# Optimization experiments

Measured on AMD Instinct MI355X. Metric: run time of the kernel, lower is better.

## Reference

```python
import jax, jax.numpy as jnp
import numpy as np
from jax import lax

D, H, B, T = 128, 256, 64, 2048

def setup_inputs() -> dict:
    key = jax.random.key(0)
    k1, k2, k3, k4 = jax.random.split(key, 4)
    s_ih = 1.0 / np.sqrt(D)
    s_hh = 1.0 / np.sqrt(H)
    return {
        "inputs": jax.random.normal(k1, (B, T, D), dtype=jnp.float32),
        "W_ih": jax.random.normal(k2, (D, 4 * H), dtype=jnp.float32) * s_ih,
        "W_hh": jax.random.normal(k3, (H, 4 * H), dtype=jnp.float32) * s_hh,
        "b": jnp.zeros((4 * H,), dtype=jnp.float32),
        "W_out": jax.random.normal(k4, (H, 1), dtype=jnp.float32) * s_hh,
        "b_out": jnp.zeros((1,), dtype=jnp.float32),
    }

def _lstm_last_h(x_bt, W_ih, W_hh, b):
    # x_bt: [B, T, D] -> time-major [T, B, D]
    x = jnp.transpose(x_bt, (1, 0, 2))
    # precompute input projections as one big GEMM: [T, B, 4H]
    x_proj = jnp.einsum('tbd,dg->tbg', x, W_ih) + b
    nb = x.shape[1]
    h0 = jnp.zeros((nb, W_hh.shape[0]), dtype=x.dtype)
    c0 = jnp.zeros_like(h0)

    def step(carry, xp):
        h, c = carry
        gates = xp + h @ W_hh            # [B, 4H]
        i, f, g, o = jnp.split(gates, 4, axis=-1)
        c = jax.nn.sigmoid(f) * c + jax.nn.sigmoid(i) * jnp.tanh(g)
        h = jax.nn.sigmoid(o) * jnp.tanh(c)
        return (h, c), None

    (h_last, _), _ = lax.scan(step, (h0, c0), x_proj)
    return h_last  # == outputs[:, -1, :]

def reference(inputs, W_ih, W_hh, b, W_out, b_out):
    h_last = _lstm_last_h(inputs, W_ih, W_hh, b)
    return h_last @ W_out + b_out  # [B, 1]
```

## Files before the change

kernel.cpp:

```cpp
#include <hip/hip_runtime.h>
#include <math.h>

#define D   128
#define H   256
#define G4  1024
#define B   64
#define T   2048

__device__ __forceinline__ float fast_sig(float x) {
    return 1.0f / (1.0f + __expf(-x));
}
__device__ __forceinline__ float fast_tanh(float x) {
    float a = __expf(-2.0f * fabsf(x));
    float r = (1.0f - a) / (1.0f + a);
    return copysignf(r, x);
}
__device__ __forceinline__ void fma4(float4& s, float a, const float4 w) {
    s.x = fmaf(a, w.x, s.x);
    s.y = fmaf(a, w.y, s.y);
    s.z = fmaf(a, w.z, s.z);
    s.w = fmaf(a, w.w, s.w);
}

__global__ __launch_bounds__(256) void lstm_xproj(
    const float* __restrict__ x, const float* __restrict__ Wih,
    float* __restrict__ xp, int t0, int tn)
{
    const int bi  = blockIdx.x % B;
    const int tt0 = (blockIdx.x / B) * 16;
    const int tid = threadIdx.x;

    __shared__ float4 xt[16][32];

    const float4* src = (const float4*)(x + ((size_t)bi * T + (size_t)(t0 + tt0)) * D);
    #pragma unroll
    for (int r = tid; r < 16 * 32; r += 256) ((float4*)xt)[r] = src[r];
    __syncthreads();

    const float4* W4 = (const float4*)Wih;
    float4 acc[16];
    #pragma unroll
    for (int tt = 0; tt < 16; ++tt) acc[tt] = make_float4(0.f, 0.f, 0.f, 0.f);

    for (int k0 = 0; k0 < 32; ++k0) {
        const int k = 4 * k0;
        float4 w0 = W4[(k + 0) * 256 + tid];
        float4 w1 = W4[(k + 1) * 256 + tid];
        float4 w2 = W4[(k + 2) * 256 + tid];
        float4 w3 = W4[(k + 3) * 256 + tid];
        #pragma unroll
        for (int tt = 0; tt < 16; ++tt) {
            float4 xv = xt[tt][k0];
            fma4(acc[tt], xv.x, w0);
            fma4(acc[tt], xv.y, w1);
            fma4(acc[tt], xv.z, w2);
            fma4(acc[tt], xv.w, w3);
        }
    }
    #pragma unroll
    for (int tt = 0; tt < 16; ++tt) {
        ((float4*)(xp + ((size_t)(tt0 + tt) * B + bi) * G4))[tid] = acc[tt];
    }
}

template <bool INLINE_X>
__global__ __launch_bounds__(1024) void lstm_scan(
    const float* __restrict__ x,  const float* __restrict__ xp,
    const float* __restrict__ Wih, const float* __restrict__ Whh,
    const float* __restrict__ bias, const float* __restrict__ Wout,
    const float* __restrict__ bout,
    float* __restrict__ hstate, float* __restrict__ cstate,
    float* __restrict__ out, int t0, int tn)
{
    const int b   = blockIdx.x;
    const int tid = threadIdx.x;
    const int c4  = tid >> 2;
    const int ks  = tid & 3;

    __shared__ float h_lds[H];
    __shared__ float gates[G4];
    __shared__ float xrow[2][D];
    __shared__ float red[4];

    float c_reg = 0.f, bi_ = 0.f, bf_ = 0.f, bg_ = 0.f, bo_ = 0.f, wout = 0.f;
    if (tid < H) {
        if (t0 == 0) {
            h_lds[tid] = 0.f;
            c_reg = 0.f;
        } else {
            h_lds[tid] = hstate[b * H + tid];
            c_reg      = cstate[b * H + tid];
        }
        bi_  = bias[tid];
        bf_  = bias[H + tid];
        bg_  = bias[2 * H + tid];
        bo_  = bias[3 * H + tid];
        wout = Wout[tid];
    }
    if (INLINE_X) {
        if (tid < D / 4) {
            ((float4*)xrow[0])[tid] =
                ((const float4*)(x + ((size_t)b * T + t0) * D))[tid];
        }
    }
    __syncthreads();

    const float4* Whh4 = (const float4*)Whh;
    const float4* Wih4 = (const float4*)Wih;
    const float4* h4   = (const float4*)h_lds;

    float4 xp_cur = make_float4(0.f, 0.f, 0.f, 0.f);
    float4 xp_nxt = make_float4(0.f, 0.f, 0.f, 0.f);
    if (!INLINE_X && ks == 0)
        xp_cur = ((const float4*)(xp + ((size_t)0 * B + b) * G4))[c4];

    for (int i = 0; i < tn; ++i) {
        float4 s = make_float4(0.f, 0.f, 0.f, 0.f);

        if (!INLINE_X) {
            if (ks == 0 && (i + 1) < tn)
                xp_nxt = ((const float4*)(xp + ((size_t)(i + 1) * B + b) * G4))[c4];
            if (ks == 0) s = xp_cur;
        } else {
            const float* xr = xrow[i & 1];
            #pragma unroll 2
            for (int k0 = 0; k0 < 8; ++k0) {
                const int k = 32 * ks + 4 * k0;
                float4 xv = *(const float4*)&xr[k];
                float4 w0 = Wih4[(k + 0) * 256 + c4];
                float4 w1 = Wih4[(k + 1) * 256 + c4];
                float4 w2 = Wih4[(k + 2) * 256 + c4];
                float4 w3 = Wih4[(k + 3) * 256 + c4];
                fma4(s, xv.x, w0);
                fma4(s, xv.y, w1);
                fma4(s, xv.z, w2);
                fma4(s, xv.w, w3);
            }
            if (tid < 32 && (i + 1) < tn) {
                ((float4*)xrow[(i + 1) & 1])[tid] =
                    ((const float4*)(x + ((size_t)b * T + (size_t)(t0 + i + 1)) * D))[tid];
            }
        }

        #pragma unroll 4
        for (int k0 = 0; k0 < 16; ++k0) {
            const int kb = 16 * ks + k0;
            float4 hv = h4[kb];
            const int k = 4 * kb;
            float4 w0 = Whh4[(k + 0) * 256 + c4];
            float4 w1 = Whh4[(k + 1) * 256 + c4];
            float4 w2 = Whh4[(k + 2) * 256 + c4];
            float4 w3 = Whh4[(k + 3) * 256 + c4];
            fma4(s, hv.x, w0);
            fma4(s, hv.y, w1);
            fma4(s, hv.z, w2);
            fma4(s, hv.w, w3);
        }

        s.x += __shfl_xor(s.x, 1); s.x += __shfl_xor(s.x, 2);
        s.y += __shfl_xor(s.y, 1); s.y += __shfl_xor(s.y, 2);
        s.z += __shfl_xor(s.z, 1); s.z += __shfl_xor(s.z, 2);
        s.w += __shfl_xor(s.w, 1); s.w += __shfl_xor(s.w, 2);
        if (ks == 0) ((float4*)gates)[c4] = s;
        __syncthreads();

        if (tid < H) {
            const int j = tid;
            float gi = gates[j]         + bi_;
            float gf = gates[H + j]     + bf_;
            float gg = gates[2 * H + j] + bg_;
            float go = gates[3 * H + j] + bo_;
            c_reg = fast_sig(gf) * c_reg + fast_sig(gi) * fast_tanh(gg);
            float hn = fast_sig(go) * fast_tanh(c_reg);
            h_lds[j] = hn;
        }
        __syncthreads();

        xp_cur = xp_nxt;
    }

    if (t0 + tn < T) {
        if (tid < H) {
            hstate[b * H + tid] = h_lds[tid];
            cstate[b * H + tid] = c_reg;
        }
    } else {
        if (tid < H) {
            float p = h_lds[tid] * wout;
            #pragma unroll
            for (int m = 32; m >= 1; m >>= 1) p += __shfl_xor(p, m);
            if ((tid & 63) == 0) red[tid >> 6] = p;
        }
        __syncthreads();
        if (tid == 0) out[b] = red[0] + red[1] + red[2] + red[3] + bout[0];
    }
}

extern "C" void kernel_launch(void* const* d_in, const int* in_sizes, int n_in,
                              void* d_out, int out_size, void* d_ws, size_t ws_size,
                              hipStream_t stream)
{
    const float* x    = (const float*)d_in[0];
    const float* Wih  = (const float*)d_in[1];
    const float* Whh  = (const float*)d_in[2];
    const float* bias = (const float*)d_in[3];
    const float* Wout = (const float*)d_in[4];
    const float* bout = (const float*)d_in[5];
    float* out = (float*)d_out;

    const size_t state_bytes = (size_t)2 * B * H * sizeof(float);

    int chunkT = 0;
    for (int c = T; c >= 16; c >>= 1) {
        if ((size_t)c * B * G4 * sizeof(float) + state_bytes <= ws_size) {
            chunkT = c;
            break;
        }
    }

    if (chunkT == 0) {
        lstm_scan<true><<<B, 1024, 0, stream>>>(
            x, nullptr, Wih, Whh, bias, Wout, bout,
            nullptr, nullptr, out, 0, T);
    } else {
        float* xp = (float*)d_ws;
        float* hs = (float*)((char*)d_ws + (size_t)chunkT * B * G4 * sizeof(float));
        float* cs = hs + B * H;
        for (int t0 = 0; t0 < T; t0 += chunkT) {
            lstm_xproj<<<dim3((chunkT / 16) * B), 256, 0, stream>>>(
                x, Wih, xp, t0, chunkT);
            lstm_scan<false><<<B, 1024, 0, stream>>>(
                x, xp, Wih, Whh, bias, Wout, bout,
                hs, cs, out, t0, chunkT);
        }
    }
}
```

Before: 60.63 ms.

## Interleave gate weights so each thread computes all four gates of one unit

Adds a repack kernel that interleaves the i/f/g/o columns of W_ih, W_hh and the bias, so one float4 holds all four gates for a hidden unit. The scan kernel drops from 1024 threads with a 4-way k-split, shuffle reduction and shared gates buffer to 256 threads. Each thread now computes the full dot product for its unit and applies the cell update in registers. It double-buffers h in LDS to need one barrier per step and prefetches weight rows into a register ring. This removes the shuffle reduction and one sync per step, but each thread streams 4x more weight data from L2 per step with less parallelism to hide latency.

Measured after the change: 67.80 ms. 1.12x slower.

```diff
diff --git a/kernel.cpp b/kernel.cpp
--- a/kernel.cpp
+++ b/kernel.cpp
@@ -22,8 +22,31 @@
     s.w = fmaf(a, w.w, s.w);
 }
 
+__global__ __launch_bounds__(256) void lstm_repack(
+    const float* __restrict__ Wih, const float* __restrict__ Whh,
+    const float* __restrict__ bias,
+    float* __restrict__ Wihp, float* __restrict__ Whhp,
+    float* __restrict__ biasp)
+{
+    const int r = blockIdx.x;
+    const int c = threadIdx.x;
+    if (r < H) {
+        const float* src = Whh + (size_t)r * G4;
+        float4 v = make_float4(src[c], src[H + c], src[2 * H + c], src[3 * H + c]);
+        ((float4*)(Whhp + (size_t)r * G4))[c] = v;
+    } else if (r < H + D) {
+        const int d = r - H;
+        const float* src = Wih + (size_t)d * G4;
+        float4 v = make_float4(src[c], src[H + c], src[2 * H + c], src[3 * H + c]);
+        ((float4*)(Wihp + (size_t)d * G4))[c] = v;
+    } else {
+        float4 v = make_float4(bias[c], bias[H + c], bias[2 * H + c], bias[3 * H + c]);
+        ((float4*)biasp)[c] = v;
+    }
+}
+
 __global__ __launch_bounds__(256) void lstm_xproj(
-    const float* __restrict__ x, const float* __restrict__ Wih,
+    const float* __restrict__ x, const float* __restrict__ Wihp,
     float* __restrict__ xp, int t0, int tn)
 {
     const int bi  = blockIdx.x % B;
@@ -37,7 +60,7 @@
     for (int r = tid; r < 16 * 32; r += 256) ((float4*)xt)[r] = src[r];
     __syncthreads();
 
-    const float4* W4 = (const float4*)Wih;
+    const float4* W4 = (const float4*)Wihp;
     float4 acc[16];
     #pragma unroll
     for (int tt = 0; tt < 16; ++tt) acc[tt] = make_float4(0.f, 0.f, 0.f, 0.f);
@@ -64,135 +87,131 @@
 }
 
 template <bool INLINE_X>
-__global__ __launch_bounds__(1024) void lstm_scan(
+__global__ __launch_bounds__(256, 1) void lstm_scan3(
     const float* __restrict__ x,  const float* __restrict__ xp,
-    const float* __restrict__ Wih, const float* __restrict__ Whh,
-    const float* __restrict__ bias, const float* __restrict__ Wout,
+    const float* __restrict__ Wihp, const float* __restrict__ Whhp,
+    const float* __restrict__ biasp, const float* __restrict__ Wout,
     const float* __restrict__ bout,
     float* __restrict__ hstate, float* __restrict__ cstate,
     float* __restrict__ out, int t0, int tn)
 {
-    const int b   = blockIdx.x;
-    const int tid = threadIdx.x;
-    const int c4  = tid >> 2;
-    const int ks  = tid & 3;
-
-    __shared__ float h_lds[H];
-    __shared__ float gates[G4];
+    const int b = blockIdx.x;
+    const int c = threadIdx.x;
+
+    __shared__ float h_lds[2][H];
     __shared__ float xrow[2][D];
     __shared__ float red[4];
 
-    float c_reg = 0.f, bi_ = 0.f, bf_ = 0.f, bg_ = 0.f, bo_ = 0.f, wout = 0.f;
-    if (tid < H) {
-        if (t0 == 0) {
-            h_lds[tid] = 0.f;
-            c_reg = 0.f;
+    const float4 bz = ((const float4*)biasp)[c];
+    const float wout = Wout[c];
+
+    float c_reg;
+    if (t0 == 0) {
+        h_lds[0][c] = 0.f;
+        c_reg = 0.f;
+    } else {
+        h_lds[0][c] = hstate[b * H + c];
+        c_reg       = cstate[b * H + c];
+    }
+    if (INLINE_X) {
+        if (c < D / 4) {
+            ((float4*)xrow[0])[c] =
+                ((const float4*)(x + ((size_t)b * T + t0) * D))[c];
+        }
+    }
+    __syncthreads();
+
+    const float4* W   = (const float4*)Whhp;
+    const float4* Wx  = (const float4*)Wihp;
+    const float4* xp4 = (const float4*)xp;
+
+    float4 xpn = make_float4(0.f, 0.f, 0.f, 0.f);
+    if (!INLINE_X) xpn = xp4[((size_t)0 * B + b) * 256 + c];
+
+    int cur = 0;
+    for (int i = 0; i < tn; ++i) {
+        float4 acc;
+        if (!INLINE_X) {
+            acc = make_float4(xpn.x + bz.x, xpn.y + bz.y, xpn.z + bz.z, xpn.w + bz.w);
+            if (i + 1 < tn)
+                xpn = xp4[((size_t)(i + 1) * B + b) * 256 + c];
         } else {
-            h_lds[tid] = hstate[b * H + tid];
-            c_reg      = cstate[b * H + tid];
-        }
-        bi_  = bias[tid];
-        bf_  = bias[H + tid];
-        bg_  = bias[2 * H + tid];
-        bo_  = bias[3 * H + tid];
-        wout = Wout[tid];
-    }
-    if (INLINE_X) {
-        if (tid < D / 4) {
-            ((float4*)xrow[0])[tid] =
-                ((const float4*)(x + ((size_t)b * T + t0) * D))[tid];
-        }
-    }
-    __syncthreads();
-
-    const float4* Whh4 = (const float4*)Whh;
-    const float4* Wih4 = (const float4*)Wih;
-    const float4* h4   = (const float4*)h_lds;
-
-    float4 xp_cur = make_float4(0.f, 0.f, 0.f, 0.f);
-    float4 xp_nxt = make_float4(0.f, 0.f, 0.f, 0.f);
-    if (!INLINE_X && ks == 0)
-        xp_cur = ((const float4*)(xp + ((size_t)0 * B + b) * G4))[c4];
-
-    for (int i = 0; i < tn; ++i) {
-        float4 s = make_float4(0.f, 0.f, 0.f, 0.f);
-
-        if (!INLINE_X) {
-            if (ks == 0 && (i + 1) < tn)
-                xp_nxt = ((const float4*)(xp + ((size_t)(i + 1) * B + b) * G4))[c4];
-            if (ks == 0) s = xp_cur;
-        } else {
+            acc = bz;
             const float* xr = xrow[i & 1];
-            #pragma unroll 2
+            const float4* xr4 = (const float4*)xr;
+            float4 wst[2][16];
+            #pragma unroll
+            for (int j = 0; j < 16; ++j) wst[0][j] = Wx[(size_t)j * 256 + c];
+            #pragma unroll
             for (int k0 = 0; k0 < 8; ++k0) {
-                const int k = 32 * ks + 4 * k0;
-                float4 xv = *(const float4*)&xr[k];
-                float4 w0 = Wih4[(k + 0) * 256 + c4];
-                float4 w1 = Wih4[(k + 1) * 256 + c4];
-                float4 w2 = Wih4[(k + 2) * 256 + c4];
-                float4 w3 = Wih4[(k + 3) * 256 + c4];
-                fma4(s, xv.x, w0);
-                fma4(s, xv.y, w1);
-                fma4(s, xv.z, w2);
-                fma4(s, xv.w, w3);
+                const int cb = k0 & 1, nb = cb ^ 1;
+                if (k0 < 7) {
+                    #pragma unroll
+                    for (int j = 0; j < 16; ++j)
+                        wst[nb][j] = Wx[(size_t)((k0 + 1) * 16 + j) * 256 + c];
+                }
+                float4 q0 = xr4[k0 * 4 + 0], q1 = xr4[k0 * 4 + 1];
+                float4 q2 = xr4[k0 * 4 + 2], q3 = xr4[k0 * 4 + 3];
+                fma4(acc, q0.x, wst[cb][0]);  fma4(acc, q0.y, wst[cb][1]);
+                fma4(acc, q0.z, wst[cb][2]);  fma4(acc, q0.w, wst[cb][3]);
+                fma4(acc, q1.x, wst[cb][4]);  fma4(acc, q1.y, wst[cb][5]);
+                fma4(acc, q1.z, wst[cb][6]);  fma4(acc, q1.w, wst[cb][7]);
+                fma4(acc, q2.x, wst[cb][8]);  fma4(acc, q2.y, wst[cb][9]);
+                fma4(acc, q2.z, wst[cb][10]); fma4(acc, q2.w, wst[cb][11]);
+                fma4(acc, q3.x, wst[cb][12]); fma4(acc, q3.y, wst[cb][13]);
+                fma4(acc, q3.z, wst[cb][14]); fma4(acc, q3.w, wst[cb][15]);
             }
-            if (tid < 32 && (i + 1) < tn) {
-                ((float4*)xrow[(i + 1) & 1])[tid] =
-                    ((const float4*)(x + ((size_t)b * T + (size_t)(t0 + i + 1)) * D))[tid];
+            if (c < D / 4 && (i + 1) < tn) {
+                ((float4*)xrow[(i + 1) & 1])[c] =
+                    ((const float4*)(x + ((size_t)b * T + (size_t)(t0 + i + 1)) * D))[c];
             }
         }
 
-        #pragma unroll 4
-        for (int k0 = 0; k0 < 16; ++k0) {
-            const int kb = 16 * ks + k0;
-            float4 hv = h4[kb];
-            const int k = 4 * kb;
-            float4 w0 = Whh4[(k + 0) * 256 + c4];
-            float4 w1 = Whh4[(k + 1) * 256 + c4];
-            float4 w2 = Whh4[(k + 2) * 256 + c4];
-            float4 w3 = Whh4[(k + 3) * 256 + c4];
-            fma4(s, hv.x, w0);
-            fma4(s, hv.y, w1);
-            fma4(s, hv.z, w2);
-            fma4(s, hv.w, w3);
-        }
-
-        s.x += __shfl_xor(s.x, 1); s.x += __shfl_xor(s.x, 2);
-        s.y += __shfl_xor(s.y, 1); s.y += __shfl_xor(s.y, 2);
-        s.z += __shfl_xor(s.z, 1); s.z += __shfl_xor(s.z, 2);
-        s.w += __shfl_xor(s.w, 1); s.w += __shfl_xor(s.w, 2);
-        if (ks == 0) ((float4*)gates)[c4] = s;
+        {
+            const float4* h4 = (const float4*)h_lds[cur];
+            float4 wst[2][16];
+            #pragma unroll
+            for (int j = 0; j < 16; ++j) wst[0][j] = W[(size_t)j * 256 + c];
+            #pragma unroll
+            for (int k0 = 0; k0 < 16; ++k0) {
+                const int cb = k0 & 1, nb = cb ^ 1;
+                if (k0 < 15) {
+                    #pragma unroll
+                    for (int j = 0; j < 16; ++j)
+                        wst[nb][j] = W[(size_t)((k0 + 1) * 16 + j) * 256 + c];
+                }
+                float4 q0 = h4[k0 * 4 + 0], q1 = h4[k0 * 4 + 1];
+                float4 q2 = h4[k0 * 4 + 2], q3 = h4[k0 * 4 + 3];
+                fma4(acc, q0.x, wst[cb][0]);  fma4(acc, q0.y, wst[cb][1]);
+                fma4(acc, q0.z, wst[cb][2]);  fma4(acc, q0.w, wst[cb][3]);
+                fma4(acc, q1.x, wst[cb][4]);  fma4(acc, q1.y, wst[cb][5]);
+                fma4(acc, q1.z, wst[cb][6]);  fma4(acc, q1.w, wst[cb][7]);
+                fma4(acc, q2.x, wst[cb][8]);  fma4(acc, q2.y, wst[cb][9]);
+                fma4(acc, q2.z, wst[cb][10]); fma4(acc, q2.w, wst[cb][11]);
+                fma4(acc, q3.x, wst[cb][12]); fma4(acc, q3.y, wst[cb][13]);
+                fma4(acc, q3.z, wst[cb][14]); fma4(acc, q3.w, wst[cb][15]);
+            }
+        }
+
+        float ct = fast_sig(acc.y) * c_reg + fast_sig(acc.x) * fast_tanh(acc.z);
+        float hn = fast_sig(acc.w) * fast_tanh(ct);
+        c_reg = ct;
+        const int nxt = cur ^ 1;
+        h_lds[nxt][c] = hn;
         __syncthreads();
-
-        if (tid < H) {
-            const int j = tid;
-            float gi = gates[j]         + bi_;
-            float gf = gates[H + j]     + bf_;
-            float gg = gates[2 * H + j] + bg_;
-            float go = gates[3 * H + j] + bo_;
-            c_reg = fast_sig(gf) * c_reg + fast_sig(gi) * fast_tanh(gg);
-            float hn = fast_sig(go) * fast_tanh(c_reg);
-            h_lds[j] = hn;
-        }
+        cur = nxt;
+    }
+
+    if (t0 + tn < T) {
+        hstate[b * H + c] = h_lds[cur][c];
+        cstate[b * H + c] = c_reg;
+    } else {
+        float p = h_lds[cur][c] * wout;
+        #pragma unroll
+        for (int m = 32; m >= 1; m >>= 1) p += __shfl_xor(p, m);
+        if ((c & 63) == 0) red[c >> 6] = p;
         __syncthreads();
-
-        xp_cur = xp_nxt;
-    }
-
-    if (t0 + tn < T) {
-        if (tid < H) {
-            hstate[b * H + tid] = h_lds[tid];
-            cstate[b * H + tid] = c_reg;
-        }
-    } else {
-        if (tid < H) {
-            float p = h_lds[tid] * wout;
-            #pragma unroll
-            for (int m = 32; m >= 1; m >>= 1) p += __shfl_xor(p, m);
-            if ((tid & 63) == 0) red[tid >> 6] = p;
-        }
-        __syncthreads();
-        if (tid == 0) out[b] = red[0] + red[1] + red[2] + red[3] + bout[0];
+        if (c == 0) out[b] = red[0] + red[1] + red[2] + red[3] + bout[0];
     }
 }
 
@@ -208,29 +227,33 @@
     const float* bout = (const float*)d_in[5];
     float* out = (float*)d_out;
 
-    const size_t state_bytes = (size_t)2 * B * H * sizeof(float);
+    char* p = (char*)d_ws;
+    float* Whhp  = (float*)p;  p += (size_t)H * G4 * sizeof(float);
+    float* Wihp  = (float*)p;  p += (size_t)D * G4 * sizeof(float);
+    float* biasp = (float*)p;  p += (size_t)G4 * sizeof(float);
+    float* hs    = (float*)p;  p += (size_t)B * H * sizeof(float);
+    float* cs    = (float*)p;  p += (size_t)B * H * sizeof(float);
+    float* xp    = (float*)p;
+    const size_t used = (size_t)(p - (char*)d_ws);
+    const size_t rem  = (ws_size > used) ? ws_size - used : 0;
 
     int chunkT = 0;
-    for (int c = T; c >= 16; c >>= 1) {
-        if ((size_t)c * B * G4 * sizeof(float) + state_bytes <= ws_size) {
-            chunkT = c;
-            break;
-        }
-    }
+    for (int ct = T; ct >= 16; ct >>= 1) {
+        if ((size_t)ct * B * G4 * sizeof(float) <= rem) { chunkT = ct; break; }
+    }
+
+    lstm_repack<<<H + D + 1, 256, 0, stream>>>(Wih, Whh, bias, Wihp, Whhp, biasp);
 
     if (chunkT == 0) {
-        lstm_scan<true><<<B, 1024, 0, stream>>>(
-            x, nullptr, Wih, Whh, bias, Wout, bout,
-            nullptr, nullptr, out, 0, T);
-    } else {
-        float* xp = (float*)d_ws;
-        float* hs = (float*)((char*)d_ws + (size_t)chunkT * B * G4 * sizeof(float));
-        float* cs = hs + B * H;
+        lstm_scan3<true><<<B, 256, 0, stream>>>(
+            x, nullptr, Wihp, Whhp, biasp, Wout, bout,
+            hs, cs, out, 0, T);
+    } else {
         for (int t0 = 0; t0 < T; t0 += chunkT) {
             lstm_xproj<<<dim3((chunkT / 16) * B), 256, 0, stream>>>(
-                x, Wih, xp, t0, chunkT);
-            lstm_scan<false><<<B, 1024, 0, stream>>>(
-                x, xp, Wih, Whh, bias, Wout, bout,
+                x, Wihp, xp, t0, chunkT);
+            lstm_scan3<false><<<B, 256, 0, stream>>>(
+                x, xp, Wihp, Whhp, biasp, Wout, bout,
                 hs, cs, out, t0, chunkT);
         }
     }
```

## Store recurrent weights as bf16 with gate-interleaved layout and split-K scan

Applied to the files above, without the earlier changes.

Adds a repack kernel that converts W_hh to bf16 and interleaves the four gates per hidden unit, and permutes W_ih and bias the same way. The scan kernel is rewritten so each of four thread groups handles a quarter of the reduction over K for all 256 units. Partial sums are combined through LDS instead of shuffles, and weight loads are double-buffered in registers. This halves the per-step weight bandwidth on the serial recurrence at the cost of bf16 rounding error accumulated over 2048 steps.

Measured after the change: 51.82 ms. 1.17x faster.

```diff
diff --git a/kernel.cpp b/kernel.cpp
--- a/kernel.cpp
+++ b/kernel.cpp
@@ -1,4 +1,5 @@
 #include <hip/hip_runtime.h>
+#include <hip/hip_bf16.h>
 #include <math.h>
 
 #define D   128
@@ -22,8 +23,54 @@
     s.w = fmaf(a, w.w, s.w);
 }
 
+__device__ __forceinline__ float bf_lo(unsigned v) {
+    union { unsigned u; float f; } t; t.u = v << 16; return t.f;
+}
+__device__ __forceinline__ float bf_hi(unsigned v) {
+    union { unsigned u; float f; } t; t.u = v & 0xFFFF0000u; return t.f;
+}
+__device__ __forceinline__ void fma_bf(float4& s, float a, const uint2 w) {
+    s.x = fmaf(a, bf_lo(w.x), s.x);
+    s.y = fmaf(a, bf_hi(w.x), s.y);
+    s.z = fmaf(a, bf_lo(w.y), s.z);
+    s.w = fmaf(a, bf_hi(w.y), s.w);
+}
+__device__ __forceinline__ unsigned short bfround(float x) {
+    __hip_bfloat16 h = __float2bfloat16(x);
+    union { __hip_bfloat16 b; unsigned short u; } t; t.b = h; return t.u;
+}
+
+__global__ __launch_bounds__(256) void lstm_repack(
+    const float* __restrict__ Wih, const float* __restrict__ Whh,
+    const float* __restrict__ bias,
+    float* __restrict__ Wihp, uint2* __restrict__ Whhb,
+    float* __restrict__ biasp)
+{
+    const int r = blockIdx.x;
+    const int c = threadIdx.x;
+    if (r < H) {
+        const float* src = Whh + (size_t)r * G4;
+        unsigned wi = bfround(src[c]);
+        unsigned wf = bfround(src[H + c]);
+        unsigned wg = bfround(src[2 * H + c]);
+        unsigned wo = bfround(src[3 * H + c]);
+        uint2 v;
+        v.x = (wf << 16) | wi;
+        v.y = (wo << 16) | wg;
+        Whhb[(size_t)r * 256 + c] = v;
+    } else if (r < H + D) {
+        const int d = r - H;
+        const float* src = Wih + (size_t)d * G4;
+        float4 v = make_float4(src[c], src[H + c], src[2 * H + c], src[3 * H + c]);
+        ((float4*)(Wihp + (size_t)d * G4))[c] = v;
+    } else {
+        float4 v = make_float4(bias[c], bias[H + c], bias[2 * H + c], bias[3 * H + c]);
+        ((float4*)biasp)[c] = v;
+    }
+}
+
 __global__ __launch_bounds__(256) void lstm_xproj(
-    const float* __restrict__ x, const float* __restrict__ Wih,
+    const float* __restrict__ x, const float* __restrict__ Wihp,
     float* __restrict__ xp, int t0, int tn)
 {
     const int bi  = blockIdx.x % B;
@@ -37,7 +84,7 @@
     for (int r = tid; r < 16 * 32; r += 256) ((float4*)xt)[r] = src[r];
     __syncthreads();
 
-    const float4* W4 = (const float4*)Wih;
+    const float4* W4 = (const float4*)Wihp;
     float4 acc[16];
     #pragma unroll
     for (int tt = 0; tt < 16; ++tt) acc[tt] = make_float4(0.f, 0.f, 0.f, 0.f);
@@ -63,14 +110,118 @@
     }
 }
 
-template <bool INLINE_X>
-__global__ __launch_bounds__(1024) void lstm_scan(
-    const float* __restrict__ x,  const float* __restrict__ xp,
-    const float* __restrict__ Wih, const float* __restrict__ Whh,
-    const float* __restrict__ bias, const float* __restrict__ Wout,
+__global__ __launch_bounds__(1024, 4) void lstm_scan7(
+    const float* __restrict__ xp, const uint2* __restrict__ Whhb,
+    const float* __restrict__ biasp, const float* __restrict__ Wout,
     const float* __restrict__ bout,
     float* __restrict__ hstate, float* __restrict__ cstate,
     float* __restrict__ out, int t0, int tn)
+{
+    const int b   = blockIdx.x;
+    const int tid = threadIdx.x;
+    const int c   = tid & 255;
+    const int ks  = tid >> 8;
+
+    __shared__ __align__(16) float hbuf[2][H];
+    __shared__ float4 part[4][H];
+    __shared__ float red[4];
+
+    float c_reg = 0.f;
+    float4 bz = make_float4(0.f, 0.f, 0.f, 0.f);
+    if (ks == 0) {
+        bz = ((const float4*)biasp)[c];
+        if (t0 == 0) {
+            hbuf[0][c] = 0.f;
+            c_reg = 0.f;
+        } else {
+            hbuf[0][c] = hstate[b * H + c];
+            c_reg      = cstate[b * H + c];
+        }
+    }
+    __syncthreads();
+
+    const float4* xp4 = (const float4*)xp;
+
+    float4 xpn = make_float4(0.f, 0.f, 0.f, 0.f);
+    if (ks == 0) xpn = xp4[((size_t)0 * B + b) * 256 + c];
+
+    const int rbase = 64 * ks;
+    int cur = 0;
+    for (int i = 0; i < tn; ++i) {
+        float4 acc;
+        if (ks == 0) {
+            acc = make_float4(xpn.x + bz.x, xpn.y + bz.y,
+                              xpn.z + bz.z, xpn.w + bz.w);
+            if (i + 1 < tn)
+                xpn = xp4[((size_t)(i + 1) * B + b) * 256 + c];
+        } else {
+            acc = make_float4(0.f, 0.f, 0.f, 0.f);
+        }
+
+        {
+            const float4* hq = (const float4*)(hbuf[cur] + rbase);
+            uint2 wst[2][8];
+            #pragma unroll
+            for (int jj = 0; jj < 8; ++jj)
+                wst[0][jj] = Whhb[(size_t)(rbase + jj) * 256 + c];
+            #pragma unroll
+            for (int j0 = 0; j0 < 8; ++j0) {
+                const int cb = j0 & 1, nb = cb ^ 1;
+                if (j0 < 7) {
+                    #pragma unroll
+                    for (int jj = 0; jj < 8; ++jj)
+                        wst[nb][jj] =
+                            Whhb[(size_t)(rbase + (j0 + 1) * 8 + jj) * 256 + c];
+                }
+                float4 h0 = hq[j0 * 2 + 0];
+                float4 h1 = hq[j0 * 2 + 1];
+                fma_bf(acc, h0.x, wst[cb][0]); fma_bf(acc, h0.y, wst[cb][1]);
+                fma_bf(acc, h0.z, wst[cb][2]); fma_bf(acc, h0.w, wst[cb][3]);
+                fma_bf(acc, h1.x, wst[cb][4]); fma_bf(acc, h1.y, wst[cb][5]);
+                fma_bf(acc, h1.z, wst[cb][6]); fma_bf(acc, h1.w, wst[cb][7]);
+            }
+        }
+
+        part[ks][c] = acc;
+        __syncthreads();
+
+        if (ks == 0) {
+            float4 p1 = part[1][c], p2 = part[2][c], p3 = part[3][c];
+            float gi = acc.x + p1.x + p2.x + p3.x;
+            float gf = acc.y + p1.y + p2.y + p3.y;
+            float gg = acc.z + p1.z + p2.z + p3.z;
+            float go = acc.w + p1.w + p2.w + p3.w;
+            float ct = fast_sig(gf) * c_reg + fast_sig(gi) * fast_tanh(gg);
+            float hn = fast_sig(go) * fast_tanh(ct);
+            c_reg = ct;
+            hbuf[cur ^ 1][c] = hn;
+        }
+        __syncthreads();
+        cur ^= 1;
+    }
+
+    if (t0 + tn < T) {
+        if (ks == 0) {
+            hstate[b * H + c] = hbuf[cur][c];
+            cstate[b * H + c] = c_reg;
+        }
+    } else {
+        if (tid < H) {
+            float p = hbuf[cur][tid] * Wout[tid];
+            #pragma unroll
+            for (int m = 32; m >= 1; m >>= 1) p += __shfl_xor(p, m);
+            if ((tid & 63) == 0) red[tid >> 6] = p;
+        }
+        __syncthreads();
+        if (tid == 0) out[b] = red[0] + red[1] + red[2] + red[3] + bout[0];
+    }
+}
+
+__global__ __launch_bounds__(1024) void lstm_scan_fused(
+    const float* __restrict__ x, const float* __restrict__ Wih,
+    const float* __restrict__ Whh, const float* __restrict__ bias,
+    const float* __restrict__ Wout, const float* __restrict__ bout,
+    float* __restrict__ out)
 {
     const int b   = blockIdx.x;
     const int tid = threadIdx.x;
@@ -82,118 +233,66 @@
     __shared__ float xrow[2][D];
     __shared__ float red[4];
 
-    float c_reg = 0.f, bi_ = 0.f, bf_ = 0.f, bg_ = 0.f, bo_ = 0.f, wout = 0.f;
+    float c_reg = 0.f, bi_ = 0.f, bf_ = 0.f, bg_ = 0.f, bo_ = 0.f;
     if (tid < H) {
-        if (t0 == 0) {
-            h_lds[tid] = 0.f;
-            c_reg = 0.f;
-        } else {
-            h_lds[tid] = hstate[b * H + tid];
-            c_reg      = cstate[b * H + tid];
-        }
-        bi_  = bias[tid];
-        bf_  = bias[H + tid];
-        bg_  = bias[2 * H + tid];
-        bo_  = bias[3 * H + tid];
-        wout = Wout[tid];
-    }
-    if (INLINE_X) {
-        if (tid < D / 4) {
-            ((float4*)xrow[0])[tid] =
-                ((const float4*)(x + ((size_t)b * T + t0) * D))[tid];
-        }
-    }
+        h_lds[tid] = 0.f;
+        bi_ = bias[tid];       bf_ = bias[H + tid];
+        bg_ = bias[2 * H + tid]; bo_ = bias[3 * H + tid];
+    }
+    if (tid < D / 4)
+        ((float4*)xrow[0])[tid] = ((const float4*)(x + (size_t)b * T * D))[tid];
     __syncthreads();
 
     const float4* Whh4 = (const float4*)Whh;
     const float4* Wih4 = (const float4*)Wih;
     const float4* h4   = (const float4*)h_lds;
 
-    float4 xp_cur = make_float4(0.f, 0.f, 0.f, 0.f);
-    float4 xp_nxt = make_float4(0.f, 0.f, 0.f, 0.f);
-    if (!INLINE_X && ks == 0)
-        xp_cur = ((const float4*)(xp + ((size_t)0 * B + b) * G4))[c4];
-
-    for (int i = 0; i < tn; ++i) {
+    for (int i = 0; i < T; ++i) {
         float4 s = make_float4(0.f, 0.f, 0.f, 0.f);
-
-        if (!INLINE_X) {
-            if (ks == 0 && (i + 1) < tn)
-                xp_nxt = ((const float4*)(xp + ((size_t)(i + 1) * B + b) * G4))[c4];
-            if (ks == 0) s = xp_cur;
-        } else {
-            const float* xr = xrow[i & 1];
-            #pragma unroll 2
-            for (int k0 = 0; k0 < 8; ++k0) {
-                const int k = 32 * ks + 4 * k0;
-                float4 xv = *(const float4*)&xr[k];
-                float4 w0 = Wih4[(k + 0) * 256 + c4];
-                float4 w1 = Wih4[(k + 1) * 256 + c4];
-                float4 w2 = Wih4[(k + 2) * 256 + c4];
-                float4 w3 = Wih4[(k + 3) * 256 + c4];
-                fma4(s, xv.x, w0);
-                fma4(s, xv.y, w1);
-                fma4(s, xv.z, w2);
-                fma4(s, xv.w, w3);
-            }
-            if (tid < 32 && (i + 1) < tn) {
-                ((float4*)xrow[(i + 1) & 1])[tid] =
-                    ((const float4*)(x + ((size_t)b * T + (size_t)(t0 + i + 1)) * D))[tid];
-            }
-        }
-
+        const float* xr = xrow[i & 1];
+        for (int k0 = 0; k0 < 8; ++k0) {
+            const int k = 32 * ks + 4 * k0;
+            float4 xv = *(const float4*)&xr[k];
+            fma4(s, xv.x, Wih4[(k + 0) * 256 + c4]);
+            fma4(s, xv.y, Wih4[(k + 1) * 256 + c4]);
+            fma4(s, xv.z, Wih4[(k + 2) * 256 + c4]);
+            fma4(s, xv.w, Wih4[(k + 3) * 256 + c4]);
+        }
+        if (tid < 32 && (i + 1) < T)
+            ((float4*)xrow[(i + 1) & 1])[tid] =
+                ((const float4*)(x + ((size_t)b * T + i + 1) * D))[tid];
         #pragma unroll 4
         for (int k0 = 0; k0 < 16; ++k0) {
             const int kb = 16 * ks + k0;
             float4 hv = h4[kb];
             const int k = 4 * kb;
-            float4 w0 = Whh4[(k + 0) * 256 + c4];
-            float4 w1 = Whh4[(k + 1) * 256 + c4];
-            float4 w2 = Whh4[(k + 2) * 256 + c4];
-            float4 w3 = Whh4[(k + 3) * 256 + c4];
-            fma4(s, hv.x, w0);
-            fma4(s, hv.y, w1);
-            fma4(s, hv.z, w2);
-            fma4(s, hv.w, w3);
-        }
-
+            fma4(s, hv.x, Whh4[(k + 0) * 256 + c4]);
+            fma4(s, hv.y, Whh4[(k + 1) * 256 + c4]);
+            fma4(s, hv.z, Whh4[(k + 2) * 256 + c4]);
+            fma4(s, hv.w, Whh4[(k + 3) * 256 + c4]);
+        }
         s.x += __shfl_xor(s.x, 1); s.x += __shfl_xor(s.x, 2);
         s.y += __shfl_xor(s.y, 1); s.y += __shfl_xor(s.y, 2);
         s.z += __shfl_xor(s.z, 1); s.z += __shfl_xor(s.z, 2);
         s.w += __shfl_xor(s.w, 1); s.w += __shfl_xor(s.w, 2);
         if (ks == 0) ((float4*)gates)[c4] = s;
         __syncthreads();
-
         if (tid < H) {
-            const int j = tid;
-            float gi = gates[j]         + bi_;
-            float gf = gates[H + j]     + bf_;
-            float gg = gates[2 * H + j] + bg_;
-            float go = gates[3 * H + j] + bo_;
+            float gi = gates[tid] + bi_, gf = gates[H + tid] + bf_;
+            float gg = gates[2 * H + tid] + bg_, go = gates[3 * H + tid] + bo_;
             c_reg = fast_sig(gf) * c_reg + fast_sig(gi) * fast_tanh(gg);
-            float hn = fast_sig(go) * fast_tanh(c_reg);
-            h_lds[j] = hn;
-        }
-        __syncthreads();
-
-        xp_cur = xp_nxt;
-    }
-
-    if (t0 + tn < T) {
-        if (tid < H) {
-            hstate[b * H + tid] = h_lds[tid];
-            cstate[b * H + tid] = c_reg;
-        }
-    } else {
-        if (tid < H) {
-            float p = h_lds[tid] * wout;
-            #pragma unroll
-            for (int m = 32; m >= 1; m >>= 1) p += __shfl_xor(p, m);
-            if ((tid & 63) == 0) red[tid >> 6] = p;
-        }
-        __syncthreads();
-        if (tid == 0) out[b] = red[0] + red[1] + red[2] + red[3] + bout[0];
-    }
+            h_lds[tid] = fast_sig(go) * fast_tanh(c_reg);
+        }
+        __syncthreads();
+    }
+    if (tid < H) {
+        float p = h_lds[tid] * Wout[tid];
+        #pragma unroll
+        for (int m = 32; m >= 1; m >>= 1) p += __shfl_xor(p, m);
+        if ((tid & 63) == 0) red[tid >> 6] = p;
+    }
+    __syncthreads();
+    if (tid == 0) out[b] = red[0] + red[1] + red[2] + red[3] + bout[0];
 }
 
 extern "C" void kernel_launch(void* const* d_in, const int* in_sizes, int n_in,
@@ -208,30 +307,34 @@
     const float* bout = (const float*)d_in[5];
     float* out = (float*)d_out;
 
-    const size_t state_bytes = (size_t)2 * B * H * sizeof(float);
+    char* p = (char*)d_ws;
+    uint2* Whhb  = (uint2*)p;  p += (size_t)H * 256 * sizeof(uint2);
+    float* Wihp  = (float*)p;  p += (size_t)D * G4 * sizeof(float);
+    float* biasp = (float*)p;  p += (size_t)G4 * sizeof(float);
+    float* hs    = (float*)p;  p += (size_t)B * H * sizeof(float);
+    float* cs    = (float*)p;  p += (size_t)B * H * sizeof(float);
+    float* xp    = (float*)p;
+    const size_t used = (size_t)(p - (char*)d_ws);
+    const size_t rem  = (ws_size > used) ? ws_size - used : 0;
 
     int chunkT = 0;
-    for (int c = T; c >= 16; c >>= 1) {
-        if ((size_t)c * B * G4 * sizeof(float) + state_bytes <= ws_size) {
-            chunkT = c;
-            break;
-        }
+    for (int ct = T; ct >= 16; ct >>= 1) {
+        if ((size_t)ct * B * G4 * sizeof(float) <= rem) { chunkT = ct; break; }
     }
 
     if (chunkT == 0) {
-        lstm_scan<true><<<B, 1024, 0, stream>>>(
-            x, nullptr, Wih, Whh, bias, Wout, bout,
-            nullptr, nullptr, out, 0, T);
-    } else {
-        float* xp = (float*)d_ws;
-        float* hs = (float*)((char*)d_ws + (size_t)chunkT * B * G4 * sizeof(float));
-        float* cs = hs + B * H;
-        for (int t0 = 0; t0 < T; t0 += chunkT) {
-            lstm_xproj<<<dim3((chunkT / 16) * B), 256, 0, stream>>>(
-                x, Wih, xp, t0, chunkT);
-            lstm_scan<false><<<B, 1024, 0, stream>>>(
-                x, xp, Wih, Whh, bias, Wout, bout,
-                hs, cs, out, t0, chunkT);
-        }
-    }
-}
+        lstm_scan_fused<<<B, 1024, 0, stream>>>(
+            x, Wih, Whh, bias, Wout, bout, out);
+        return;
+    }
+
+    lstm_repack<<<H + D + 1, 256, 0, stream>>>(Wih, Whh, bias, Wihp, Whhb, biasp);
+
+    for (int t0 = 0; t0 < T; t0 += chunkT) {
+        lstm_xproj<<<dim3((chunkT / 16) * B), 256, 0, stream>>>(
+            x, Wihp, xp, t0, chunkT);
+        lstm_scan7<<<B, 1024, 0, stream>>>(
+            xp, Whhb, biasp, Wout, bout,
+            hs, cs, out, t0, chunkT);
+    }
+}
```
